# Kernel optimization log

Hardware: AMD Instinct MI355X
Metric: run time of the kernel (lower is better)

## Reference

```python
import jax, jax.numpy as jnp
import numpy as np


def setup_inputs() -> dict:
    key = jax.random.key(0)
    kx, ky = jax.random.split(key)
    B, SX, SY, D = 8, 2048, 2048, 512
    x = jax.random.normal(kx, (B, SX, D), dtype=jnp.float32)
    y = jax.random.normal(ky, (B, SY, D), dtype=jnp.float32)
    return {"x": x, "y": y}


def reference(x, y):
    # e = x @ y^T : [B, Sx, Sy]
    e = jnp.einsum("bsd,btd->bst", x, y)
    ai = jax.nn.softmax(e, axis=-1)
    # a = ai @ y : [B, Sx, D]
    a = jnp.einsum("bst,btd->bsd", ai, y)
    # concat [x, a] along feature dim -> [B, Sx, 2D]; dropout in eval mode = identity
    out = jnp.concatenate([x, a], axis=-1)
    return out
```

## Files before the change

### kernel.cpp

```cpp
#include <hip/hip_runtime.h>
#include <stdint.h>

typedef _Float16 half4v __attribute__((ext_vector_type(4)));
typedef _Float16 half8v __attribute__((ext_vector_type(8)));
typedef float    f32x4  __attribute__((ext_vector_type(4)));
typedef __attribute__((address_space(3))) void       lds_void;
typedef const __attribute__((address_space(1))) void g_void;

#define NB 8
#define SXX 2048
#define DD 512
#define QBLK 64
#define TBLK 64
#define NITER 32

#define RSB 1040u
#define BUFSZ (64u * RSB)
#define POFF  (2u * BUFSZ)
#define PR    136u
#define SCOFF (POFF + 64u * PR)
#define TMOFF (SCOFF + 256u)
#define LOFF  (TMOFF + 512u)
#define LDS_BYTES 143104
#define YH_BYTES (8ull * 2048ull * 512ull * 2ull)

__global__ __launch_bounds__(256)
void convert_y(const float* __restrict__ y, _Float16* __restrict__ yh) {
  const int i = (blockIdx.x * 256 + threadIdx.x) * 8;
  f32x4 f0 = *(const f32x4*)(y + i);
  f32x4 f1 = *(const f32x4*)(y + i + 4);
  half8v h;
  h[0]=(_Float16)f0[0]; h[1]=(_Float16)f0[1]; h[2]=(_Float16)f0[2]; h[3]=(_Float16)f0[3];
  h[4]=(_Float16)f1[0]; h[5]=(_Float16)f1[1]; h[6]=(_Float16)f1[2]; h[7]=(_Float16)f1[3];
  *(half8v*)(yh + i) = h;
}

template <bool USE_WS>
__global__ __launch_bounds__(512, 2)
void attn_fused(const float* __restrict__ x, const float* __restrict__ y,
                const _Float16* __restrict__ yh, float* __restrict__ out) {
  extern __shared__ char smem[];
  const int bid   = blockIdx.x;
  const int b     = bid & 7;
  const int qtile = bid >> 3;
  const int tid   = threadIdx.x;
  const int w     = tid >> 6;
  const int lane  = tid & 63;
  const int l15   = lane & 15;
  const int g     = lane >> 4;
  const int qw    = w & 3;
  const int th    = w >> 2;

  const float*    xb  = x + (size_t)b * SXX * DD;
  const float*    yb  = y + (size_t)b * SXX * DD;
  const _Float16* yhb = USE_WS ? (yh + (size_t)b * SXX * DD) : nullptr;
  float* outb = out + (size_t)b * SXX * (2 * DD);
  const int qbase = qtile * QBLK;

  if (USE_WS) {
#pragma unroll
    for (int i = 0; i < 8; ++i) {
      const int row = w * 8 + i;
      __builtin_amdgcn_global_load_lds((g_void*)(yhb + row * DD + lane * 8),
                                       (lds_void*)(smem + (uint32_t)row * RSB), 16, 0, 0);
    }
  }

  {
    const f32x4* src = (const f32x4*)(xb + (size_t)qbase * DD);
    for (int i = tid; i < QBLK * (DD / 4); i += 512) {
      f32x4 v = src[i];
      *(f32x4*)(outb + (size_t)(qbase + (i >> 7)) * (2 * DD) + (i & 127) * 4) = v;
    }
  }

  half8v bq[16];
  {
    const float* xr = xb + (size_t)(qbase + qw * 16 + l15) * DD;
#pragma unroll
    for (int c = 0; c < 16; ++c) {
      const int d0 = c * 32 + g * 8;
      f32x4 f0 = *(const f32x4*)(xr + d0);
      f32x4 f1 = *(const f32x4*)(xr + d0 + 4);
      half8v h;
      h[0] = (_Float16)f0[0]; h[1] = (_Float16)f0[1];
      h[2] = (_Float16)f0[2]; h[3] = (_Float16)f0[3];
      h[4] = (_Float16)f1[0]; h[5] = (_Float16)f1[1];
      h[6] = (_Float16)f1[2]; h[7] = (_Float16)f1[3];
      bq[c] = h;
    }
  }

  if (!USE_WS) {
#pragma unroll
    for (int k = 0; k < 8; ++k) {
      const int u = tid + k * 512;
      const int t = u >> 6, c8 = u & 63;
      const float* p = yb + t * DD + c8 * 8;
      f32x4 f0 = *(const f32x4*)p, f1 = *(const f32x4*)(p + 4);
      half8v h;
      h[0]=(_Float16)f0[0]; h[1]=(_Float16)f0[1]; h[2]=(_Float16)f0[2]; h[3]=(_Float16)f0[3];
      h[4]=(_Float16)f1[0]; h[5]=(_Float16)f1[1]; h[6]=(_Float16)f1[2]; h[7]=(_Float16)f1[3];
      *(half8v*)(smem + (uint32_t)t * RSB + (uint32_t)c8 * 16u) = h;
    }
  }

  f32x4 acc[4][4];
#pragma unroll
  for (int i = 0; i < 4; ++i)
#pragma unroll
    for (int j = 0; j < 4; ++j) acc[i][j] = (f32x4){0.f, 0.f, 0.f, 0.f};
  float mrun = -3.0e38f, lrun = 0.0f;

  __syncthreads();

  for (int it = 0; it < NITER; ++it) {
    const uint32_t cb  = (uint32_t)(it & 1) * BUFSZ;
    const uint32_t nb2 = cb ^ BUFSZ;

    if (USE_WS && it + 1 < NITER) {
      const _Float16* src = yhb + (size_t)(it + 1) * TBLK * DD;
#pragma unroll
      for (int i = 0; i < 8; ++i) {
        const int row = w * 8 + i;
        __builtin_amdgcn_global_load_lds((g_void*)(src + row * DD + lane * 8),
                                         (lds_void*)(smem + nb2 + (uint32_t)row * RSB), 16, 0, 0);
      }
    }

    f32x4 st[2];
    st[0] = (f32x4){0.f, 0.f, 0.f, 0.f};
    st[1] = (f32x4){0.f, 0.f, 0.f, 0.f};
#pragma unroll
    for (int c = 0; c < 16; ++c) {
      const uint32_t db = cb + 64u * (uint32_t)c + 16u * (uint32_t)g;
#pragma unroll
      for (int tt = 0; tt < 2; ++tt) {
        const half8v af =
            *(const half8v*)(smem + (uint32_t)(th * 32 + tt * 16 + l15) * RSB + db);
        st[tt] = __builtin_amdgcn_mfma_f32_16x16x32_f16(af, bq[c], st[tt], 0, 0, 0);
      }
    }

    float tmax = -3.0e38f;
#pragma unroll
    for (int tt = 0; tt < 2; ++tt)
#pragma unroll
      for (int r = 0; r < 4; ++r) tmax = fmaxf(tmax, st[tt][r]);
    tmax = fmaxf(tmax, __shfl_xor(tmax, 16));
    tmax = fmaxf(tmax, __shfl_xor(tmax, 32));
    if (g == 0) ((float*)(smem + TMOFF))[th * 64 + qw * 16 + l15] = tmax;
    __syncthreads();
    const float tm0 = ((float*)(smem + TMOFF))[qw * 16 + l15];
    const float tm1 = ((float*)(smem + TMOFF))[64 + qw * 16 + l15];
    const float mnew = fmaxf(mrun, fmaxf(tm0, tm1));

    float pvv[8];
    float rsum = 0.f;
#pragma unroll
    for (int tt = 0; tt < 2; ++tt)
#pragma unroll
      for (int r = 0; r < 4; ++r) {
        const float e = __expf(st[tt][r] - mnew);
        pvv[tt * 4 + r] = e;
        rsum += e;
      }
    rsum += __shfl_xor(rsum, 16);
    rsum += __shfl_xor(rsum, 32);
    const float scale = __expf(mrun - mnew);
    lrun = lrun * scale + rsum;
    mrun = mnew;

#pragma unroll
    for (int tt = 0; tt < 2; ++tt) {
      half4v hv;
      hv[0] = (_Float16)pvv[tt * 4 + 0]; hv[1] = (_Float16)pvv[tt * 4 + 1];
      hv[2] = (_Float16)pvv[tt * 4 + 2]; hv[3] = (_Float16)pvv[tt * 4 + 3];
      *(half4v*)(smem + POFF + (uint32_t)(qw * 16 + l15) * PR +
                 (uint32_t)(th * 64 + tt * 32) + (uint32_t)g * 8u) = hv;
    }
    if (th == 0 && g == 0) ((float*)(smem + SCOFF))[qw * 16 + l15] = scale;

    if (!USE_WS && it + 1 < NITER) {
      const float* ybt = yb + (size_t)(it + 1) * TBLK * DD;
#pragma unroll
      for (int k = 0; k < 8; ++k) {
        const int u = tid + k * 512;
        const int t = u >> 6, c8 = u & 63;
        const float* p = ybt + t * DD + c8 * 8;
        f32x4 f0 = *(const f32x4*)p, f1 = *(const f32x4*)(p + 4);
        half8v h;
        h[0]=(_Float16)f0[0]; h[1]=(_Float16)f0[1]; h[2]=(_Float16)f0[2]; h[3]=(_Float16)f0[3];
        h[4]=(_Float16)f1[0]; h[5]=(_Float16)f1[1]; h[6]=(_Float16)f1[2]; h[7]=(_Float16)f1[3];
        *(half8v*)(smem + nb2 + (uint32_t)t * RSB + (uint32_t)c8 * 16u) = h;
      }
    }

    __syncthreads();

    {
#pragma unroll
      for (int qq = 0; qq < 4; ++qq) {
        const f32x4 s4 = *(const f32x4*)(smem + SCOFF + (uint32_t)(qq * 16 + 4 * g) * 4u);
#pragma unroll
        for (int dtl = 0; dtl < 4; ++dtl) {
          acc[qq][dtl][0] *= s4[0]; acc[qq][dtl][1] *= s4[1];
          acc[qq][dtl][2] *= s4[2]; acc[qq][dtl][3] *= s4[3];
        }
      }
      __builtin_amdgcn_sched_barrier(0);

      half4v palo[4][2], pahi[4][2];
      const uint32_t pb = POFF + (uint32_t)l15 * PR + (uint32_t)g * 8u;
#pragma unroll
      for (int qq = 0; qq < 4; ++qq)
#pragma unroll
        for (int ch = 0; ch < 2; ++ch) {
          const uint32_t a = pb + (uint32_t)qq * (16u * PR) + (uint32_t)ch * 64u;
          asm volatile("ds_read_b64 %0, %1" : "=v"(palo[qq][ch]) : "v"(a));
          asm volatile("ds_read_b64 %0, %1" : "=v"(pahi[qq][ch]) : "v"(a + 32u));
        }
      half4v blo[8], bhi[8];
      const uint32_t tb = cb + (uint32_t)(4 * g + (l15 >> 2)) * RSB +
                          (uint32_t)(l15 & 3) * 8u + (uint32_t)w * 128u;
#pragma unroll
      for (int fr = 0; fr < 8; ++fr) {
        const uint32_t a = tb + (uint32_t)(fr >> 2) * (32u * RSB) + (uint32_t)(fr & 3) * 32u;
        asm volatile("ds_read_b64_tr_b16 %0, %1" : "=v"(blo[fr]) : "v"(a));
        asm volatile("ds_read_b64_tr_b16 %0, %1" : "=v"(bhi[fr]) : "v"(a + 16u * RSB));
      }
      asm volatile("s_waitcnt lgkmcnt(0)" ::: "memory");
      __builtin_amdgcn_sched_barrier(0);

#pragma unroll
      for (int fr = 0; fr < 8; ++fr) {
        const half8v b8 = __builtin_shufflevector(blo[fr], bhi[fr], 0, 1, 2, 3, 4, 5, 6, 7);
        const int ch = fr >> 2, dtl = fr & 3;
#pragma unroll
        for (int qq = 0; qq < 4; ++qq) {
          const half8v pa = __builtin_shufflevector(palo[qq][ch], pahi[qq][ch],
                                                    0, 1, 2, 3, 4, 5, 6, 7);
          acc[qq][dtl] = __builtin_amdgcn_mfma_f32_16x16x32_f16(pa, b8, acc[qq][dtl], 0, 0, 0);
        }
      }
    }
    __syncthreads();
  }

  if (g == 0) ((float*)(smem + LOFF))[th * 64 + qw * 16 + l15] = lrun;
  __syncthreads();
#pragma unroll
  for (int qq = 0; qq < 4; ++qq) {
    const f32x4 l0 = *(const f32x4*)(smem + LOFF + (uint32_t)(qq * 16 + 4 * g) * 4u);
    const f32x4 l1 = *(const f32x4*)(smem + LOFF + 256u + (uint32_t)(qq * 16 + 4 * g) * 4u);
    f32x4 iv;
#pragma unroll
    for (int r = 0; r < 4; ++r) iv[r] = 1.0f / (l0[r] + l1[r]);
#pragma unroll
    for (int dtl = 0; dtl < 4; ++dtl) {
#pragma unroll
      for (int r = 0; r < 4; ++r) {
        const int q = qbase + qq * 16 + 4 * g + r;
        outb[(size_t)q * (2 * DD) + DD + w * 64 + dtl * 16 + l15] = acc[qq][dtl][r] * iv[r];
      }
    }
  }
}

extern "C" void kernel_launch(void* const* d_in, const int* in_sizes, int n_in,
                              void* d_out, int out_size, void* d_ws, size_t ws_size,
                              hipStream_t stream) {
  (void)in_sizes; (void)n_in; (void)out_size;
  const float* x = (const float*)d_in[0];
  const float* y = (const float*)d_in[1];
  float* out = (float*)d_out;
  static_assert(LDS_BYTES <= 160 * 1024, "LDS over budget");
  const bool use_ws = (ws_size >= YH_BYTES);
  if (use_ws) {
    _Float16* yh = (_Float16*)d_ws;
    hipLaunchKernelGGL(convert_y, dim3(4096), dim3(256), 0, stream, y, yh);
    hipFuncSetAttribute((const void*)attn_fused<true>,
                        hipFuncAttributeMaxDynamicSharedMemorySize, LDS_BYTES);
    hipLaunchKernelGGL((attn_fused<true>), dim3((SXX / QBLK) * NB), dim3(512),
                       LDS_BYTES, stream, x, y, yh, out);
  } else {
    hipFuncSetAttribute((const void*)attn_fused<false>,
                        hipFuncAttributeMaxDynamicSharedMemorySize, LDS_BYTES);
    hipLaunchKernelGGL((attn_fused<false>), dim3((SXX / QBLK) * NB), dim3(512),
                       LDS_BYTES, stream, x, y, nullptr, out);
  }
}
```

Before: 115.6 us.

## Repartition QK^T warps to 2 query groups x 4 key slices, reuse key fragments

The QK^T phase now splits the 8 waves into 2 query groups of 32 rows by 4 key slices of 16, instead of 4 query groups by 2 key slices. Each wave loads a key fragment once and reuses it for two query MFMAs, so the per-iteration LDS reads of Y in the score phase are halved. The cost is twice as many query registers (bq0/bq1), a 4-way max and sum reduction through LDS, and a slightly larger LDS budget. The PV phase is also split into two chunks with separate waits, which lowers peak register pressure.

```diff
diff --git a/kernel.cpp b/kernel.cpp
--- a/kernel.cpp
+++ b/kernel.cpp
@@ -20,8 +20,8 @@
 #define PR    136u
 #define SCOFF (POFF + 64u * PR)
 #define TMOFF (SCOFF + 256u)
-#define LOFF  (TMOFF + 512u)
-#define LDS_BYTES 143104
+#define LOFF  (TMOFF + 1024u)
+#define LDS_BYTES 144128
 #define YH_BYTES (8ull * 2048ull * 512ull * 2ull)
 
 __global__ __launch_bounds__(256)
@@ -48,8 +48,8 @@
   const int lane  = tid & 63;
   const int l15   = lane & 15;
   const int g     = lane >> 4;
-  const int qw    = w & 3;
-  const int th    = w >> 2;
+  const int qg    = w & 1;
+  const int tq    = w >> 1;
 
   const float*    xb  = x + (size_t)b * SXX * DD;
   const float*    yb  = y + (size_t)b * SXX * DD;
@@ -74,20 +74,24 @@
     }
   }
 
-  half8v bq[16];
+  half8v bq0[16], bq1[16];
   {
-    const float* xr = xb + (size_t)(qbase + qw * 16 + l15) * DD;
+    const float* xr0 = xb + (size_t)(qbase + qg * 32 + l15) * DD;
+    const float* xr1 = xr0 + 16 * DD;
 #pragma unroll
     for (int c = 0; c < 16; ++c) {
       const int d0 = c * 32 + g * 8;
-      f32x4 f0 = *(const f32x4*)(xr + d0);
-      f32x4 f1 = *(const f32x4*)(xr + d0 + 4);
+      f32x4 f0 = *(const f32x4*)(xr0 + d0);
+      f32x4 f1 = *(const f32x4*)(xr0 + d0 + 4);
       half8v h;
-      h[0] = (_Float16)f0[0]; h[1] = (_Float16)f0[1];
-      h[2] = (_Float16)f0[2]; h[3] = (_Float16)f0[3];
-      h[4] = (_Float16)f1[0]; h[5] = (_Float16)f1[1];
-      h[6] = (_Float16)f1[2]; h[7] = (_Float16)f1[3];
-      bq[c] = h;
+      h[0]=(_Float16)f0[0]; h[1]=(_Float16)f0[1]; h[2]=(_Float16)f0[2]; h[3]=(_Float16)f0[3];
+      h[4]=(_Float16)f1[0]; h[5]=(_Float16)f1[1]; h[6]=(_Float16)f1[2]; h[7]=(_Float16)f1[3];
+      bq0[c] = h;
+      f0 = *(const f32x4*)(xr1 + d0);
+      f1 = *(const f32x4*)(xr1 + d0 + 4);
+      h[0]=(_Float16)f0[0]; h[1]=(_Float16)f0[1]; h[2]=(_Float16)f0[2]; h[3]=(_Float16)f0[3];
+      h[4]=(_Float16)f1[0]; h[5]=(_Float16)f1[1]; h[6]=(_Float16)f1[2]; h[7]=(_Float16)f1[3];
+      bq1[c] = h;
     }
   }
 
@@ -110,7 +114,7 @@
   for (int i = 0; i < 4; ++i)
 #pragma unroll
     for (int j = 0; j < 4; ++j) acc[i][j] = (f32x4){0.f, 0.f, 0.f, 0.f};
-  float mrun = -3.0e38f, lrun = 0.0f;
+  float mrun0 = -3.0e38f, mrun1 = -3.0e38f, lrun0 = 0.0f, lrun1 = 0.0f;
 
   __syncthreads();
 
@@ -128,58 +132,58 @@
       }
     }
 
-    f32x4 st[2];
-    st[0] = (f32x4){0.f, 0.f, 0.f, 0.f};
-    st[1] = (f32x4){0.f, 0.f, 0.f, 0.f};
+    f32x4 st0 = (f32x4){0.f, 0.f, 0.f, 0.f};
+    f32x4 st1 = (f32x4){0.f, 0.f, 0.f, 0.f};
 #pragma unroll
     for (int c = 0; c < 16; ++c) {
-      const uint32_t db = cb + 64u * (uint32_t)c + 16u * (uint32_t)g;
-#pragma unroll
-      for (int tt = 0; tt < 2; ++tt) {
-        const half8v af =
-            *(const half8v*)(smem + (uint32_t)(th * 32 + tt * 16 + l15) * RSB + db);
-        st[tt] = __builtin_amdgcn_mfma_f32_16x16x32_f16(af, bq[c], st[tt], 0, 0, 0);
-      }
-    }
-
-    float tmax = -3.0e38f;
-#pragma unroll
-    for (int tt = 0; tt < 2; ++tt)
-#pragma unroll
-      for (int r = 0; r < 4; ++r) tmax = fmaxf(tmax, st[tt][r]);
-    tmax = fmaxf(tmax, __shfl_xor(tmax, 16));
-    tmax = fmaxf(tmax, __shfl_xor(tmax, 32));
-    if (g == 0) ((float*)(smem + TMOFF))[th * 64 + qw * 16 + l15] = tmax;
+      const half8v af = *(const half8v*)(smem + cb +
+          (uint32_t)(tq * 16 + l15) * RSB + 64u * (uint32_t)c + 16u * (uint32_t)g);
+      st0 = __builtin_amdgcn_mfma_f32_16x16x32_f16(af, bq0[c], st0, 0, 0, 0);
+      st1 = __builtin_amdgcn_mfma_f32_16x16x32_f16(af, bq1[c], st1, 0, 0, 0);
+    }
+
+    float tmax0 = fmaxf(fmaxf(st0[0], st0[1]), fmaxf(st0[2], st0[3]));
+    float tmax1 = fmaxf(fmaxf(st1[0], st1[1]), fmaxf(st1[2], st1[3]));
+    tmax0 = fmaxf(tmax0, __shfl_xor(tmax0, 16));
+    tmax0 = fmaxf(tmax0, __shfl_xor(tmax0, 32));
+    tmax1 = fmaxf(tmax1, __shfl_xor(tmax1, 16));
+    tmax1 = fmaxf(tmax1, __shfl_xor(tmax1, 32));
+    if (g == 0) {
+      ((float*)(smem + TMOFF))[tq * 64 + qg * 32 + l15]      = tmax0;
+      ((float*)(smem + TMOFF))[tq * 64 + qg * 32 + 16 + l15] = tmax1;
+    }
     __syncthreads();
-    const float tm0 = ((float*)(smem + TMOFF))[qw * 16 + l15];
-    const float tm1 = ((float*)(smem + TMOFF))[64 + qw * 16 + l15];
-    const float mnew = fmaxf(mrun, fmaxf(tm0, tm1));
-
-    float pvv[8];
-    float rsum = 0.f;
-#pragma unroll
-    for (int tt = 0; tt < 2; ++tt)
-#pragma unroll
-      for (int r = 0; r < 4; ++r) {
-        const float e = __expf(st[tt][r] - mnew);
-        pvv[tt * 4 + r] = e;
-        rsum += e;
-      }
-    rsum += __shfl_xor(rsum, 16);
-    rsum += __shfl_xor(rsum, 32);
-    const float scale = __expf(mrun - mnew);
-    lrun = lrun * scale + rsum;
-    mrun = mnew;
-
-#pragma unroll
-    for (int tt = 0; tt < 2; ++tt) {
+    const float* tmb = (const float*)(smem + TMOFF);
+    const int qi0 = qg * 32 + l15, qi1 = qi0 + 16;
+    const float mnew0 = fmaxf(mrun0,
+        fmaxf(fmaxf(tmb[qi0], tmb[64 + qi0]), fmaxf(tmb[128 + qi0], tmb[192 + qi0])));
+    const float mnew1 = fmaxf(mrun1,
+        fmaxf(fmaxf(tmb[qi1], tmb[64 + qi1]), fmaxf(tmb[128 + qi1], tmb[192 + qi1])));
+
+    float pv0[4], pv1[4], rs0 = 0.f, rs1 = 0.f;
+#pragma unroll
+    for (int r = 0; r < 4; ++r) {
+      pv0[r] = __expf(st0[r] - mnew0); rs0 += pv0[r];
+      pv1[r] = __expf(st1[r] - mnew1); rs1 += pv1[r];
+    }
+    rs0 += __shfl_xor(rs0, 16); rs0 += __shfl_xor(rs0, 32);
+    rs1 += __shfl_xor(rs1, 16); rs1 += __shfl_xor(rs1, 32);
+    const float scale0 = __expf(mrun0 - mnew0);
+    const float scale1 = __expf(mrun1 - mnew1);
+    lrun0 = lrun0 * scale0 + rs0;  mrun0 = mnew0;
+    lrun1 = lrun1 * scale1 + rs1;  mrun1 = mnew1;
+
+    {
       half4v hv;
-      hv[0] = (_Float16)pvv[tt * 4 + 0]; hv[1] = (_Float16)pvv[tt * 4 + 1];
-      hv[2] = (_Float16)pvv[tt * 4 + 2]; hv[3] = (_Float16)pvv[tt * 4 + 3];
-      *(half4v*)(smem + POFF + (uint32_t)(qw * 16 + l15) * PR +
-                 (uint32_t)(th * 64 + tt * 32) + (uint32_t)g * 8u) = hv;
-    }
-    if (th == 0 && g == 0) ((float*)(smem + SCOFF))[qw * 16 + l15] = scale;
+      hv[0]=(_Float16)pv0[0]; hv[1]=(_Float16)pv0[1]; hv[2]=(_Float16)pv0[2]; hv[3]=(_Float16)pv0[3];
+      *(half4v*)(smem + POFF + (uint32_t)qi0 * PR + (uint32_t)(tq * 32 + g * 8)) = hv;
+      hv[0]=(_Float16)pv1[0]; hv[1]=(_Float16)pv1[1]; hv[2]=(_Float16)pv1[2]; hv[3]=(_Float16)pv1[3];
+      *(half4v*)(smem + POFF + (uint32_t)qi1 * PR + (uint32_t)(tq * 32 + g * 8)) = hv;
+    }
+    if (tq == 0 && g == 0) {
+      ((float*)(smem + SCOFF))[qi0] = scale0;
+      ((float*)(smem + SCOFF))[qi1] = scale1;
+    }
 
     if (!USE_WS && it + 1 < NITER) {
       const float* ybt = yb + (size_t)(it + 1) * TBLK * DD;
@@ -210,52 +214,56 @@
       }
       __builtin_amdgcn_sched_barrier(0);
 
-      half4v palo[4][2], pahi[4][2];
       const uint32_t pb = POFF + (uint32_t)l15 * PR + (uint32_t)g * 8u;
-#pragma unroll
-      for (int qq = 0; qq < 4; ++qq)
-#pragma unroll
-        for (int ch = 0; ch < 2; ++ch) {
-          const uint32_t a = pb + (uint32_t)qq * (16u * PR) + (uint32_t)ch * 64u;
-          asm volatile("ds_read_b64 %0, %1" : "=v"(palo[qq][ch]) : "v"(a));
-          asm volatile("ds_read_b64 %0, %1" : "=v"(pahi[qq][ch]) : "v"(a + 32u));
-        }
-      half4v blo[8], bhi[8];
       const uint32_t tb = cb + (uint32_t)(4 * g + (l15 >> 2)) * RSB +
                           (uint32_t)(l15 & 3) * 8u + (uint32_t)w * 128u;
 #pragma unroll
-      for (int fr = 0; fr < 8; ++fr) {
-        const uint32_t a = tb + (uint32_t)(fr >> 2) * (32u * RSB) + (uint32_t)(fr & 3) * 32u;
-        asm volatile("ds_read_b64_tr_b16 %0, %1" : "=v"(blo[fr]) : "v"(a));
-        asm volatile("ds_read_b64_tr_b16 %0, %1" : "=v"(bhi[fr]) : "v"(a + 16u * RSB));
-      }
-      asm volatile("s_waitcnt lgkmcnt(0)" ::: "memory");
-      __builtin_amdgcn_sched_barrier(0);
-
-#pragma unroll
-      for (int fr = 0; fr < 8; ++fr) {
-        const half8v b8 = __builtin_shufflevector(blo[fr], bhi[fr], 0, 1, 2, 3, 4, 5, 6, 7);
-        const int ch = fr >> 2, dtl = fr & 3;
+      for (int ch = 0; ch < 2; ++ch) {
+        half4v palo[4], pahi[4];
 #pragma unroll
         for (int qq = 0; qq < 4; ++qq) {
-          const half8v pa = __builtin_shufflevector(palo[qq][ch], pahi[qq][ch],
-                                                    0, 1, 2, 3, 4, 5, 6, 7);
-          acc[qq][dtl] = __builtin_amdgcn_mfma_f32_16x16x32_f16(pa, b8, acc[qq][dtl], 0, 0, 0);
+          const uint32_t a = pb + (uint32_t)qq * (16u * PR) + (uint32_t)ch * 64u;
+          asm volatile("ds_read_b64 %0, %1" : "=v"(palo[qq]) : "v"(a));
+          asm volatile("ds_read_b64 %0, %1" : "=v"(pahi[qq]) : "v"(a + 32u));
         }
+        half4v blo[4], bhi[4];
+#pragma unroll
+        for (int dtl = 0; dtl < 4; ++dtl) {
+          const uint32_t a = tb + (uint32_t)ch * (32u * RSB) + (uint32_t)dtl * 32u;
+          asm volatile("ds_read_b64_tr_b16 %0, %1" : "=v"(blo[dtl]) : "v"(a));
+          asm volatile("ds_read_b64_tr_b16 %0, %1" : "=v"(bhi[dtl]) : "v"(a + 16u * RSB));
+        }
+        asm volatile("s_waitcnt lgkmcnt(0)" ::: "memory");
+        __builtin_amdgcn_sched_barrier(0);
+#pragma unroll
+        for (int dtl = 0; dtl < 4; ++dtl) {
+          const half8v b8 = __builtin_shufflevector(blo[dtl], bhi[dtl], 0, 1, 2, 3, 4, 5, 6, 7);
+#pragma unroll
+          for (int qq = 0; qq < 4; ++qq) {
+            const half8v pa = __builtin_shufflevector(palo[qq], pahi[qq],
+                                                      0, 1, 2, 3, 4, 5, 6, 7);
+            acc[qq][dtl] = __builtin_amdgcn_mfma_f32_16x16x32_f16(pa, b8, acc[qq][dtl], 0, 0, 0);
+          }
+        }
       }
     }
     __syncthreads();
   }
 
-  if (g == 0) ((float*)(smem + LOFF))[th * 64 + qw * 16 + l15] = lrun;
+  if (g == 0) {
+    ((float*)(smem + LOFF))[tq * 64 + qg * 32 + l15]      = lrun0;
+    ((float*)(smem + LOFF))[tq * 64 + qg * 32 + 16 + l15] = lrun1;
+  }
   __syncthreads();
 #pragma unroll
   for (int qq = 0; qq < 4; ++qq) {
     const f32x4 l0 = *(const f32x4*)(smem + LOFF + (uint32_t)(qq * 16 + 4 * g) * 4u);
     const f32x4 l1 = *(const f32x4*)(smem + LOFF + 256u + (uint32_t)(qq * 16 + 4 * g) * 4u);
+    const f32x4 l2 = *(const f32x4*)(smem + LOFF + 512u + (uint32_t)(qq * 16 + 4 * g) * 4u);
+    const f32x4 l3 = *(const f32x4*)(smem + LOFF + 768u + (uint32_t)(qq * 16 + 4 * g) * 4u);
     f32x4 iv;
 #pragma unroll
-    for (int r = 0; r < 4; ++r) iv[r] = 1.0f / (l0[r] + l1[r]);
+    for (int r = 0; r < 4; ++r) iv[r] = 1.0f / (l0[r] + l1[r] + l2[r] + l3[r]);
 #pragma unroll
     for (int dtl = 0; dtl < 4; ++dtl) {
 #pragma unroll
```

After: 140.4 us. 1.21x slower.

## Software-pipeline QK^T scores one tile ahead and drop a per-iteration barrier

Applied to the files above, without the earlier changes.

The scores MFMA and row-max for tile it+1 are now computed inside iteration it, after the accumulator rescale and before the PV matmul. A prologue computes the first tile's scores before the loop. This removes the barrier that used to sit between the score max and the softmax, and lets QK MFMAs overlap with the PV work. In exchange it raises register pressure by keeping st live across iterations. Correctness depends on the next Y buffer and the TMOFF max values being visible at the right synchronisation points.

```diff
diff --git a/kernel.cpp b/kernel.cpp
--- a/kernel.cpp
+++ b/kernel.cpp
@@ -111,7 +111,32 @@
 #pragma unroll
     for (int j = 0; j < 4; ++j) acc[i][j] = (f32x4){0.f, 0.f, 0.f, 0.f};
   float mrun = -3.0e38f, lrun = 0.0f;
-
+  f32x4 st[2];
+
+  __syncthreads();
+
+  st[0] = (f32x4){0.f, 0.f, 0.f, 0.f};
+  st[1] = (f32x4){0.f, 0.f, 0.f, 0.f};
+#pragma unroll
+  for (int c = 0; c < 16; ++c) {
+    const uint32_t db = 64u * (uint32_t)c + 16u * (uint32_t)g;
+#pragma unroll
+    for (int tt = 0; tt < 2; ++tt) {
+      const half8v af =
+          *(const half8v*)(smem + (uint32_t)(th * 32 + tt * 16 + l15) * RSB + db);
+      st[tt] = __builtin_amdgcn_mfma_f32_16x16x32_f16(af, bq[c], st[tt], 0, 0, 0);
+    }
+  }
+  {
+    float tmax = -3.0e38f;
+#pragma unroll
+    for (int tt = 0; tt < 2; ++tt)
+#pragma unroll
+      for (int r = 0; r < 4; ++r) tmax = fmaxf(tmax, st[tt][r]);
+    tmax = fmaxf(tmax, __shfl_xor(tmax, 16));
+    tmax = fmaxf(tmax, __shfl_xor(tmax, 32));
+    if (g == 0) ((float*)(smem + TMOFF))[th * 64 + qw * 16 + l15] = tmax;
+  }
   __syncthreads();
 
   for (int it = 0; it < NITER; ++it) {
@@ -128,58 +153,37 @@
       }
     }
 
-    f32x4 st[2];
-    st[0] = (f32x4){0.f, 0.f, 0.f, 0.f};
-    st[1] = (f32x4){0.f, 0.f, 0.f, 0.f};
-#pragma unroll
-    for (int c = 0; c < 16; ++c) {
-      const uint32_t db = cb + 64u * (uint32_t)c + 16u * (uint32_t)g;
+    {
+      const float* tmb = (const float*)(smem + TMOFF);
+      const float tm0 = tmb[qw * 16 + l15];
+      const float tm1 = tmb[64 + qw * 16 + l15];
+      const float mnew = fmaxf(mrun, fmaxf(tm0, tm1));
+      float pvv[8];
+      float rsum = 0.f;
+#pragma unroll
+      for (int tt = 0; tt < 2; ++tt)
+#pragma unroll
+        for (int r = 0; r < 4; ++r) {
+          const float e = __expf(st[tt][r] - mnew);
+          pvv[tt * 4 + r] = e;
+          rsum += e;
+        }
+      rsum += __shfl_xor(rsum, 16);
+      rsum += __shfl_xor(rsum, 32);
+      const float scale = __expf(mrun - mnew);
+      lrun = lrun * scale + rsum;
+      mrun = mnew;
+
 #pragma unroll
       for (int tt = 0; tt < 2; ++tt) {
-        const half8v af =
-            *(const half8v*)(smem + (uint32_t)(th * 32 + tt * 16 + l15) * RSB + db);
-        st[tt] = __builtin_amdgcn_mfma_f32_16x16x32_f16(af, bq[c], st[tt], 0, 0, 0);
-      }
-    }
-
-    float tmax = -3.0e38f;
-#pragma unroll
-    for (int tt = 0; tt < 2; ++tt)
-#pragma unroll
-      for (int r = 0; r < 4; ++r) tmax = fmaxf(tmax, st[tt][r]);
-    tmax = fmaxf(tmax, __shfl_xor(tmax, 16));
-    tmax = fmaxf(tmax, __shfl_xor(tmax, 32));
-    if (g == 0) ((float*)(smem + TMOFF))[th * 64 + qw * 16 + l15] = tmax;
-    __syncthreads();
-    const float tm0 = ((float*)(smem + TMOFF))[qw * 16 + l15];
-    const float tm1 = ((float*)(smem + TMOFF))[64 + qw * 16 + l15];
-    const float mnew = fmaxf(mrun, fmaxf(tm0, tm1));
-
-    float pvv[8];
-    float rsum = 0.f;
-#pragma unroll
-    for (int tt = 0; tt < 2; ++tt)
-#pragma unroll
-      for (int r = 0; r < 4; ++r) {
-        const float e = __expf(st[tt][r] - mnew);
-        pvv[tt * 4 + r] = e;
-        rsum += e;
-      }
-    rsum += __shfl_xor(rsum, 16);
-    rsum += __shfl_xor(rsum, 32);
-    const float scale = __expf(mrun - mnew);
-    lrun = lrun * scale + rsum;
-    mrun = mnew;
-
-#pragma unroll
-    for (int tt = 0; tt < 2; ++tt) {
-      half4v hv;
-      hv[0] = (_Float16)pvv[tt * 4 + 0]; hv[1] = (_Float16)pvv[tt * 4 + 1];
-      hv[2] = (_Float16)pvv[tt * 4 + 2]; hv[3] = (_Float16)pvv[tt * 4 + 3];
-      *(half4v*)(smem + POFF + (uint32_t)(qw * 16 + l15) * PR +
-                 (uint32_t)(th * 64 + tt * 32) + (uint32_t)g * 8u) = hv;
-    }
-    if (th == 0 && g == 0) ((float*)(smem + SCOFF))[qw * 16 + l15] = scale;
+        half4v hv;
+        hv[0] = (_Float16)pvv[tt * 4 + 0]; hv[1] = (_Float16)pvv[tt * 4 + 1];
+        hv[2] = (_Float16)pvv[tt * 4 + 2]; hv[3] = (_Float16)pvv[tt * 4 + 3];
+        *(half4v*)(smem + POFF + (uint32_t)(qw * 16 + l15) * PR +
+                   (uint32_t)(th * 64 + tt * 32) + (uint32_t)g * 8u) = hv;
+      }
+      if (th == 0 && g == 0) ((float*)(smem + SCOFF))[qw * 16 + l15] = scale;
+    }
 
     if (!USE_WS && it + 1 < NITER) {
       const float* ybt = yb + (size_t)(it + 1) * TBLK * DD;
@@ -208,8 +212,31 @@
           acc[qq][dtl][2] *= s4[2]; acc[qq][dtl][3] *= s4[3];
         }
       }
+
+      if (it + 1 < NITER) {
+        st[0] = (f32x4){0.f, 0.f, 0.f, 0.f};
+        st[1] = (f32x4){0.f, 0.f, 0.f, 0.f};
+#pragma unroll
+        for (int c = 0; c < 16; ++c) {
+          const uint32_t db = nb2 + 64u * (uint32_t)c + 16u * (uint32_t)g;
+#pragma unroll
+          for (int tt = 0; tt < 2; ++tt) {
+            const half8v af =
+                *(const half8v*)(smem + (uint32_t)(th * 32 + tt * 16 + l15) * RSB + db);
+            st[tt] = __builtin_amdgcn_mfma_f32_16x16x32_f16(af, bq[c], st[tt], 0, 0, 0);
+          }
+        }
+        float tmax = -3.0e38f;
+#pragma unroll
+        for (int tt = 0; tt < 2; ++tt)
+#pragma unroll
+          for (int r = 0; r < 4; ++r) tmax = fmaxf(tmax, st[tt][r]);
+        tmax = fmaxf(tmax, __shfl_xor(tmax, 16));
+        tmax = fmaxf(tmax, __shfl_xor(tmax, 32));
+        if (g == 0) ((float*)(smem + TMOFF))[th * 64 + qw * 16 + l15] = tmax;
+      }
+
       __builtin_amdgcn_sched_barrier(0);
-
       half4v palo[4][2], pahi[4][2];
       const uint32_t pb = POFF + (uint32_t)l15 * PR + (uint32_t)g * 8u;
 #pragma unroll
```

Measured after the change: 118.9 us. +2.9%, slower.

## Double workgroup to 16 waves, splitting key and D tiles across more waves

Applied to the files above, without the earlier changes.

The fused attention kernel now runs with 1024 threads (16 waves) instead of 512. Each wave handles one 16-key slice of the 64-key tile for QK^T and a 32-wide D slice for PV, which halves per-wave accumulator registers and MFMA work. The tile-max and row-sum reductions are extended to four key partitions, and the y-tile loading is spread over twice as many threads. This trades the previous two-blocks-per-CU occupancy for one larger block with more waves per block. It also adds more waves contending at each barrier and more LDS traffic for the reductions.

```diff
diff --git a/kernel.cpp b/kernel.cpp
--- a/kernel.cpp
+++ b/kernel.cpp
@@ -20,8 +20,8 @@
 #define PR    136u
 #define SCOFF (POFF + 64u * PR)
 #define TMOFF (SCOFF + 256u)
-#define LOFF  (TMOFF + 512u)
-#define LDS_BYTES 143104
+#define LOFF  (TMOFF + 1024u)
+#define LDS_BYTES 144128
 #define YH_BYTES (8ull * 2048ull * 512ull * 2ull)
 
 __global__ __launch_bounds__(256)
@@ -36,7 +36,7 @@
 }
 
 template <bool USE_WS>
-__global__ __launch_bounds__(512, 2)
+__global__ __launch_bounds__(1024)
 void attn_fused(const float* __restrict__ x, const float* __restrict__ y,
                 const _Float16* __restrict__ yh, float* __restrict__ out) {
   extern __shared__ char smem[];
@@ -49,7 +49,7 @@
   const int l15   = lane & 15;
   const int g     = lane >> 4;
   const int qw    = w & 3;
-  const int th    = w >> 2;
+  const int tq    = w >> 2;
 
   const float*    xb  = x + (size_t)b * SXX * DD;
   const float*    yb  = y + (size_t)b * SXX * DD;
@@ -59,8 +59,8 @@
 
   if (USE_WS) {
 #pragma unroll
-    for (int i = 0; i < 8; ++i) {
-      const int row = w * 8 + i;
+    for (int i = 0; i < 4; ++i) {
+      const int row = w * 4 + i;
       __builtin_amdgcn_global_load_lds((g_void*)(yhb + row * DD + lane * 8),
                                        (lds_void*)(smem + (uint32_t)row * RSB), 16, 0, 0);
     }
@@ -68,7 +68,7 @@
 
   {
     const f32x4* src = (const f32x4*)(xb + (size_t)qbase * DD);
-    for (int i = tid; i < QBLK * (DD / 4); i += 512) {
+    for (int i = tid; i < QBLK * (DD / 4); i += 1024) {
       f32x4 v = src[i];
       *(f32x4*)(outb + (size_t)(qbase + (i >> 7)) * (2 * DD) + (i & 127) * 4) = v;
     }
@@ -93,8 +93,8 @@
 
   if (!USE_WS) {
 #pragma unroll
-    for (int k = 0; k < 8; ++k) {
-      const int u = tid + k * 512;
+    for (int k = 0; k < 4; ++k) {
+      const int u = tid + k * 1024;
       const int t = u >> 6, c8 = u & 63;
       const float* p = yb + t * DD + c8 * 8;
       f32x4 f0 = *(const f32x4*)p, f1 = *(const f32x4*)(p + 4);
@@ -105,11 +105,12 @@
     }
   }
 
-  f32x4 acc[4][4];
-#pragma unroll
-  for (int i = 0; i < 4; ++i)
-#pragma unroll
-    for (int j = 0; j < 4; ++j) acc[i][j] = (f32x4){0.f, 0.f, 0.f, 0.f};
+  f32x4 acc[4][2];
+#pragma unroll
+  for (int i = 0; i < 4; ++i) {
+    acc[i][0] = (f32x4){0.f, 0.f, 0.f, 0.f};
+    acc[i][1] = (f32x4){0.f, 0.f, 0.f, 0.f};
+  }
   float mrun = -3.0e38f, lrun = 0.0f;
 
   __syncthreads();
@@ -121,71 +122,53 @@
     if (USE_WS && it + 1 < NITER) {
       const _Float16* src = yhb + (size_t)(it + 1) * TBLK * DD;
 #pragma unroll
-      for (int i = 0; i < 8; ++i) {
-        const int row = w * 8 + i;
+      for (int i = 0; i < 4; ++i) {
+        const int row = w * 4 + i;
         __builtin_amdgcn_global_load_lds((g_void*)(src + row * DD + lane * 8),
                                          (lds_void*)(smem + nb2 + (uint32_t)row * RSB), 16, 0, 0);
       }
     }
 
-    f32x4 st[2];
-    st[0] = (f32x4){0.f, 0.f, 0.f, 0.f};
-    st[1] = (f32x4){0.f, 0.f, 0.f, 0.f};
+    f32x4 st = (f32x4){0.f, 0.f, 0.f, 0.f};
 #pragma unroll
     for (int c = 0; c < 16; ++c) {
-      const uint32_t db = cb + 64u * (uint32_t)c + 16u * (uint32_t)g;
-#pragma unroll
-      for (int tt = 0; tt < 2; ++tt) {
-        const half8v af =
-            *(const half8v*)(smem + (uint32_t)(th * 32 + tt * 16 + l15) * RSB + db);
-        st[tt] = __builtin_amdgcn_mfma_f32_16x16x32_f16(af, bq[c], st[tt], 0, 0, 0);
-      }
-    }
-
-    float tmax = -3.0e38f;
-#pragma unroll
-    for (int tt = 0; tt < 2; ++tt)
-#pragma unroll
-      for (int r = 0; r < 4; ++r) tmax = fmaxf(tmax, st[tt][r]);
+      const half8v af = *(const half8v*)(smem + cb +
+          (uint32_t)(tq * 16 + l15) * RSB + 64u * (uint32_t)c + 16u * (uint32_t)g);
+      st = __builtin_amdgcn_mfma_f32_16x16x32_f16(af, bq[c], st, 0, 0, 0);
+    }
+
+    float tmax = fmaxf(fmaxf(st[0], st[1]), fmaxf(st[2], st[3]));
     tmax = fmaxf(tmax, __shfl_xor(tmax, 16));
     tmax = fmaxf(tmax, __shfl_xor(tmax, 32));
-    if (g == 0) ((float*)(smem + TMOFF))[th * 64 + qw * 16 + l15] = tmax;
+    if (g == 0) ((float*)(smem + TMOFF))[tq * 64 + qw * 16 + l15] = tmax;
     __syncthreads();
-    const float tm0 = ((float*)(smem + TMOFF))[qw * 16 + l15];
-    const float tm1 = ((float*)(smem + TMOFF))[64 + qw * 16 + l15];
-    const float mnew = fmaxf(mrun, fmaxf(tm0, tm1));
-
-    float pvv[8];
+    const float* tmb = (const float*)(smem + TMOFF);
+    const int qi = qw * 16 + l15;
+    const float mnew = fmaxf(mrun,
+        fmaxf(fmaxf(tmb[qi], tmb[64 + qi]), fmaxf(tmb[128 + qi], tmb[192 + qi])));
+
     float rsum = 0.f;
-#pragma unroll
-    for (int tt = 0; tt < 2; ++tt)
-#pragma unroll
-      for (int r = 0; r < 4; ++r) {
-        const float e = __expf(st[tt][r] - mnew);
-        pvv[tt * 4 + r] = e;
-        rsum += e;
-      }
+    half4v hv;
+#pragma unroll
+    for (int r = 0; r < 4; ++r) {
+      const float e = __expf(st[r] - mnew);
+      rsum += e;
+      hv[r] = (_Float16)e;
+    }
     rsum += __shfl_xor(rsum, 16);
     rsum += __shfl_xor(rsum, 32);
     const float scale = __expf(mrun - mnew);
     lrun = lrun * scale + rsum;
     mrun = mnew;
 
-#pragma unroll
-    for (int tt = 0; tt < 2; ++tt) {
-      half4v hv;
-      hv[0] = (_Float16)pvv[tt * 4 + 0]; hv[1] = (_Float16)pvv[tt * 4 + 1];
-      hv[2] = (_Float16)pvv[tt * 4 + 2]; hv[3] = (_Float16)pvv[tt * 4 + 3];
-      *(half4v*)(smem + POFF + (uint32_t)(qw * 16 + l15) * PR +
-                 (uint32_t)(th * 64 + tt * 32) + (uint32_t)g * 8u) = hv;
-    }
-    if (th == 0 && g == 0) ((float*)(smem + SCOFF))[qw * 16 + l15] = scale;
+    *(half4v*)(smem + POFF + (uint32_t)qi * PR + (uint32_t)(tq * 32 + g * 8)) = hv;
+    if (tq == 0 && g == 0) ((float*)(smem + SCOFF))[qi] = scale;
 
     if (!USE_WS && it + 1 < NITER) {
       const float* ybt = yb + (size_t)(it + 1) * TBLK * DD;
 #pragma unroll
-      for (int k = 0; k < 8; ++k) {
-        const int u = tid + k * 512;
+      for (int k = 0; k < 4; ++k) {
+        const int u = tid + k * 1024;
         const int t = u >> 6, c8 = u & 63;
         const float* p = ybt + t * DD + c8 * 8;
         f32x4 f0 = *(const f32x4*)p, f1 = *(const f32x4*)(p + 4);
@@ -203,7 +186,7 @@
       for (int qq = 0; qq < 4; ++qq) {
         const f32x4 s4 = *(const f32x4*)(smem + SCOFF + (uint32_t)(qq * 16 + 4 * g) * 4u);
 #pragma unroll
-        for (int dtl = 0; dtl < 4; ++dtl) {
+        for (int dtl = 0; dtl < 2; ++dtl) {
           acc[qq][dtl][0] *= s4[0]; acc[qq][dtl][1] *= s4[1];
           acc[qq][dtl][2] *= s4[2]; acc[qq][dtl][3] *= s4[3];
         }
@@ -220,12 +203,12 @@
           asm volatile("ds_read_b64 %0, %1" : "=v"(palo[qq][ch]) : "v"(a));
           asm volatile("ds_read_b64 %0, %1" : "=v"(pahi[qq][ch]) : "v"(a + 32u));
         }
-      half4v blo[8], bhi[8];
+      half4v blo[4], bhi[4];
       const uint32_t tb = cb + (uint32_t)(4 * g + (l15 >> 2)) * RSB +
-                          (uint32_t)(l15 & 3) * 8u + (uint32_t)w * 128u;
-#pragma unroll
-      for (int fr = 0; fr < 8; ++fr) {
-        const uint32_t a = tb + (uint32_t)(fr >> 2) * (32u * RSB) + (uint32_t)(fr & 3) * 32u;
+                          (uint32_t)(l15 & 3) * 8u + (uint32_t)w * 64u;
+#pragma unroll
+      for (int fr = 0; fr < 4; ++fr) {
+        const uint32_t a = tb + (uint32_t)(fr >> 1) * (32u * RSB) + (uint32_t)(fr & 1) * 32u;
         asm volatile("ds_read_b64_tr_b16 %0, %1" : "=v"(blo[fr]) : "v"(a));
         asm volatile("ds_read_b64_tr_b16 %0, %1" : "=v"(bhi[fr]) : "v"(a + 16u * RSB));
       }
@@ -233,9 +216,9 @@
       __builtin_amdgcn_sched_barrier(0);
 
 #pragma unroll
-      for (int fr = 0; fr < 8; ++fr) {
+      for (int fr = 0; fr < 4; ++fr) {
         const half8v b8 = __builtin_shufflevector(blo[fr], bhi[fr], 0, 1, 2, 3, 4, 5, 6, 7);
-        const int ch = fr >> 2, dtl = fr & 3;
+        const int ch = fr >> 1, dtl = fr & 1;
 #pragma unroll
         for (int qq = 0; qq < 4; ++qq) {
           const half8v pa = __builtin_shufflevector(palo[qq][ch], pahi[qq][ch],
@@ -247,21 +230,23 @@
     __syncthreads();
   }
 
-  if (g == 0) ((float*)(smem + LOFF))[th * 64 + qw * 16 + l15] = lrun;
+  if (g == 0) ((float*)(smem + LOFF))[tq * 64 + qw * 16 + l15] = lrun;
   __syncthreads();
 #pragma unroll
   for (int qq = 0; qq < 4; ++qq) {
     const f32x4 l0 = *(const f32x4*)(smem + LOFF + (uint32_t)(qq * 16 + 4 * g) * 4u);
     const f32x4 l1 = *(const f32x4*)(smem + LOFF + 256u + (uint32_t)(qq * 16 + 4 * g) * 4u);
+    const f32x4 l2 = *(const f32x4*)(smem + LOFF + 512u + (uint32_t)(qq * 16 + 4 * g) * 4u);
+    const f32x4 l3 = *(const f32x4*)(smem + LOFF + 768u + (uint32_t)(qq * 16 + 4 * g) * 4u);
     f32x4 iv;
 #pragma unroll
-    for (int r = 0; r < 4; ++r) iv[r] = 1.0f / (l0[r] + l1[r]);
-#pragma unroll
-    for (int dtl = 0; dtl < 4; ++dtl) {
+    for (int r = 0; r < 4; ++r) iv[r] = 1.0f / (l0[r] + l1[r] + l2[r] + l3[r]);
+#pragma unroll
+    for (int dtl = 0; dtl < 2; ++dtl) {
 #pragma unroll
       for (int r = 0; r < 4; ++r) {
         const int q = qbase + qq * 16 + 4 * g + r;
-        outb[(size_t)q * (2 * DD) + DD + w * 64 + dtl * 16 + l15] = acc[qq][dtl][r] * iv[r];
+        outb[(size_t)q * (2 * DD) + DD + w * 32 + dtl * 16 + l15] = acc[qq][dtl][r] * iv[r];
       }
     }
   }
@@ -281,12 +266,12 @@
     hipLaunchKernelGGL(convert_y, dim3(4096), dim3(256), 0, stream, y, yh);
     hipFuncSetAttribute((const void*)attn_fused<true>,
                         hipFuncAttributeMaxDynamicSharedMemorySize, LDS_BYTES);
-    hipLaunchKernelGGL((attn_fused<true>), dim3((SXX / QBLK) * NB), dim3(512),
+    hipLaunchKernelGGL((attn_fused<true>), dim3((SXX / QBLK) * NB), dim3(1024),
                        LDS_BYTES, stream, x, y, yh, out);
   } else {
     hipFuncSetAttribute((const void*)attn_fused<false>,
                         hipFuncAttributeMaxDynamicSharedMemorySize, LDS_BYTES);
-    hipLaunchKernelGGL((attn_fused<false>), dim3((SXX / QBLK) * NB), dim3(512),
+    hipLaunchKernelGGL((attn_fused<false>), dim3((SXX / QBLK) * NB), dim3(1024),
                        LDS_BYTES, stream, x, y, nullptr, out);
   }
 }
```

Measured after the change: 399.0 us. 245% more time.
